# Performance work log

Hardware: AMD Instinct MI355X
Metric: run time of the kernel (lower is better)

The kernel has to match this reference:

```python
import math
import jax, jax.numpy as jnp
import numpy as np

B, N, H, D = 2, 2048, 16, 64


def _build_idx_table(seq_len, is_causal=True):
    """Fused hierarchical lookup table, faithful to
    build_hierarchical_index_lookup_table. Returns int32 [seq_len, log2(N)+1].
    Entries are (node_index + 1), negated if causally masked.
    Node numbering: leaves 0..N-1, then each level's parents appended;
    parent(i) = i // 2 + seq_len.
    """
    assert seq_len & (seq_len - 1) == 0
    total_nodes = 2 * seq_len - 1
    max_valid = total_nodes - 2  # root is never a neighbor
    level_num = int(math.log2(seq_len))
    total_cols = level_num + 1
    idx = np.ones((seq_len, total_cols), dtype=np.int32)
    n_cur = np.arange(seq_len, dtype=np.int64)
    idx[:, 0] = (n_cur + 1).astype(np.int32)  # self leaf
    for lvl in range(1, total_cols):
        if lvl == 1:
            n_next = n_cur ^ 1          # sibling leaf
            pair = n_cur
        else:
            pair = n_cur // 2 + seq_len  # parent node
            n_next = pair ^ 1            # uncle node
        valid = n_next <= max_valid
        val = n_next + 1
        if is_causal:
            should_mask = (pair < n_next) & valid
            val = np.where(should_mask, -val, val)
        idx[:, lvl] = np.where(valid, val.astype(np.int32), idx[:, lvl])
        n_cur = n_next
    return idx


IDX_TABLE = _build_idx_table(N, is_causal=True)  # [N, LEVELS]


def setup_inputs() -> dict:
    key = jax.random.key(0)
    kq, kk, kv = jax.random.split(key, 3)
    Q = jax.random.normal(kq, (B, N, H, D), dtype=jnp.float32)
    K = jax.random.normal(kk, (B, N, H, D), dtype=jnp.float32)
    V = jax.random.normal(kv, (B, N, H, D), dtype=jnp.float32)
    return {"Q": Q, "K": K, "V": V}


def _build_tree(K, V, scale):
    """Build the full binary-tree node set [B, 2N-1, H, D] for K and V.
    Each parent is a 3-way attention mix of {parent-mean, child0, child1}
    (build_parent_nodes semantics: fp32 online softmax with +1e-9 in denom),
    with the same weights applied to K and V values."""
    Ks, Vs = [K], [V]
    Kc, Vc = K, V
    while Kc.shape[1] > 1:  # trace-time loop over log2(N) levels
        K0, K1 = Kc[:, 0::2], Kc[:, 1::2]
        V0, V1 = Vc[:, 0::2], Vc[:, 1::2]
        Kp0 = 0.5 * (K0 + K1)  # initial parent K (query)
        Vp0 = 0.5 * (V0 + V1)
        s_self = jnp.sum(Kp0 * Kp0, axis=-1) * scale  # [B,P,H]
        s0 = jnp.sum(Kp0 * K0, axis=-1) * scale
        s1 = jnp.sum(Kp0 * K1, axis=-1) * scale
        m = jnp.maximum(s_self, jnp.maximum(s0, s1))
        e_s, e0, e1 = jnp.exp(s_self - m), jnp.exp(s0 - m), jnp.exp(s1 - m)
        denom = e_s + e0 + e1 + 1e-9
        ws, w0, w1 = (e_s / denom)[..., None], (e0 / denom)[..., None], (e1 / denom)[..., None]
        Kc = ws * Kp0 + w0 * K0 + w1 * K1
        Vc = ws * Vp0 + w0 * V0 + w1 * V1
        Ks.append(Kc)
        Vs.append(Vc)
    return jnp.concatenate(Ks, axis=1), jnp.concatenate(Vs, axis=1)


def reference(Q, K, V):
    b, n, h, d = Q.shape
    scale = 1.0 / math.sqrt(d)
    K_all, V_all = _build_tree(K, V, scale)  # [B, 2N-1, H, D]

    raw = jnp.asarray(IDX_TABLE)             # [N, L], sign-encoded
    nbr = jnp.abs(raw) - 1                   # neighbor node indices
    masked = raw < 0                         # causal mask

    Kg = jnp.take(K_all, nbr, axis=1)        # [B, N, L, H, D]
    Vg = jnp.take(V_all, nbr, axis=1)

    scores = jnp.einsum('bnhd,bnlhd->bnhl', Q, Kg) * scale
    scores = jnp.where(masked[None, :, None, :], -jnp.inf, scores)
    w = jax.nn.softmax(scores, axis=-1)      # [B, N, H, L]
    out = jnp.einsum('bnhl,bnlhd->bnhd', w, Vg)
    return out
```

## Files before the change

kernel.cpp:

```cpp
#include <hip/hip_runtime.h>

#define NSEQ   2048
#define HEADS  16
#define DIM    64
#define BATCH  2
#define SCALE  0.125f

#define WSSLOTS 2048
#define WSELEMS ((size_t)BATCH * WSSLOTS * HEADS * DIM)
#define ROWF4   (DIM / 4)
#define HSTRIDE (HEADS * ROWF4)

__device__ __forceinline__ int level_offset(int j) {
    return (j == 0) ? 0 : (2 * NSEQ - ((2 * NSEQ) >> j));
}

__device__ __forceinline__ float dot4(float4 a, float4 b) {
    return a.x * b.x + a.y * b.y + a.z * b.z + a.w * b.w;
}

__device__ __forceinline__ void reduce3_16(float& a, float& b, float& c) {
#pragma unroll
    for (int m = 1; m < 16; m <<= 1) {
        a += __shfl_xor(a, m, 64);
        b += __shfl_xor(b, m, 64);
        c += __shfl_xor(c, m, 64);
    }
}

__device__ __forceinline__ void make_parent4(float4 k0, float4 k1, float4 v0, float4 v1,
                                             float4& kc, float4& vc) {
    float4 kp, vp;
    kp.x = 0.5f * (k0.x + k1.x); kp.y = 0.5f * (k0.y + k1.y);
    kp.z = 0.5f * (k0.z + k1.z); kp.w = 0.5f * (k0.w + k1.w);
    vp.x = 0.5f * (v0.x + v1.x); vp.y = 0.5f * (v0.y + v1.y);
    vp.z = 0.5f * (v0.z + v1.z); vp.w = 0.5f * (v0.w + v1.w);
    float ss = dot4(kp, kp), sa = dot4(kp, k0), sb = dot4(kp, k1);
    reduce3_16(ss, sa, sb);
    ss *= SCALE; sa *= SCALE; sb *= SCALE;
    float mx = fmaxf(ss, fmaxf(sa, sb));
    float es = __expf(ss - mx), ea = __expf(sa - mx), eb = __expf(sb - mx);
    float inv = 1.0f / (es + ea + eb + 1e-9f);
    es *= inv; ea *= inv; eb *= inv;
    kc.x = es * kp.x + ea * k0.x + eb * k1.x;
    kc.y = es * kp.y + ea * k0.y + eb * k1.y;
    kc.z = es * kp.z + ea * k0.z + eb * k1.z;
    kc.w = es * kp.w + ea * k0.w + eb * k1.w;
    vc.x = es * vp.x + ea * v0.x + eb * v1.x;
    vc.y = es * vp.y + ea * v0.y + eb * v1.y;
    vc.z = es * vp.z + ea * v0.z + eb * v1.z;
    vc.w = es * vp.w + ea * v0.w + eb * v1.w;
}

__global__ __launch_bounds__(256) void tree_low(const float* __restrict__ K,
                                                const float* __restrict__ V,
                                                float* __restrict__ Kw,
                                                float* __restrict__ Vw) {
    __shared__ float4 Kb[96 * ROWF4];
    __shared__ float4 Vb[96 * ROWF4];
    int c  = blockIdx.x & 15;
    int bh = blockIdx.x >> 4;
    int h  = bh & 15;
    int b  = bh >> 4;
    int wave = threadIdx.x >> 6;
    int lane = threadIdx.x & 63;
    int g = lane >> 4;
    int t = lane & 15;

    const float4* K4 = (const float4*)K;
    const float4* V4 = (const float4*)V;
    float4* Kw4 = (float4*)Kw;
    float4* Vw4 = (float4*)Vw;

#pragma unroll
    for (int j = 1; j <= 7; ++j) {
        int P = 128 >> j;
        int curOff  = (j & 1) ? 0 : 64;
        int prevOff = (j & 1) ? 64 : 0;
        for (int i0 = 0; i0 < P; i0 += 16) {
            int p = i0 + wave * 4 + g;
            if (p < P) {
                float4 k0, k1, v0, v1;
                if (j == 1) {
                    int n0 = c * 128 + 2 * p;
                    const float4* Kr = K4 + ((size_t)(b * NSEQ + n0) * HEADS + h) * ROWF4;
                    const float4* Vr = V4 + ((size_t)(b * NSEQ + n0) * HEADS + h) * ROWF4;
                    k0 = Kr[t]; k1 = Kr[HSTRIDE + t];
                    v0 = Vr[t]; v1 = Vr[HSTRIDE + t];
                } else {
                    int s = (prevOff + 2 * p) * ROWF4 + t;
                    k0 = Kb[s]; k1 = Kb[s + ROWF4];
                    v0 = Vb[s]; v1 = Vb[s + ROWF4];
                }
                float4 kc, vc;
                make_parent4(k0, k1, v0, v1, kc, vc);
                Kb[(curOff + p) * ROWF4 + t] = kc;
                Vb[(curOff + p) * ROWF4 + t] = vc;
                int slot = level_offset(j) - NSEQ + c * P + p;
                size_t widx = ((size_t)(b * WSSLOTS + slot) * HEADS + h) * ROWF4 + t;
                Kw4[widx] = kc;
                Vw4[widx] = vc;
            }
        }
        __syncthreads();
    }
}

__global__ __launch_bounds__(256) void tree_top(float* __restrict__ Kw,
                                                float* __restrict__ Vw) {
    __shared__ float4 Kb[12 * ROWF4];
    __shared__ float4 Vb[12 * ROWF4];
    int h = blockIdx.x & 15;
    int b = blockIdx.x >> 4;
    int wave = threadIdx.x >> 6;
    int lane = threadIdx.x & 63;
    int g = lane >> 4, t = lane & 15;
    int p = wave * 4 + g;

    float4* Kw4 = (float4*)Kw;
    float4* Vw4 = (float4*)Vw;

    if (p < 8) {
        int cslot = level_offset(7) - NSEQ + 2 * p;
        size_t cb = ((size_t)(b * WSSLOTS + cslot) * HEADS + h) * ROWF4 + t;
        float4 k0 = Kw4[cb], k1 = Kw4[cb + HSTRIDE];
        float4 v0 = Vw4[cb], v1 = Vw4[cb + HSTRIDE];
        float4 kc, vc;
        make_parent4(k0, k1, v0, v1, kc, vc);
        Kb[p * ROWF4 + t] = kc;  Vb[p * ROWF4 + t] = vc;
        size_t widx = ((size_t)(b * WSSLOTS + level_offset(8) - NSEQ + p) * HEADS + h) * ROWF4 + t;
        Kw4[widx] = kc;  Vw4[widx] = vc;
    }
    __syncthreads();
    if (p < 4) {
        int s = (2 * p) * ROWF4 + t;
        float4 k0 = Kb[s], k1 = Kb[s + ROWF4];
        float4 v0 = Vb[s], v1 = Vb[s + ROWF4];
        float4 kc, vc;
        make_parent4(k0, k1, v0, v1, kc, vc);
        Kb[(8 + p) * ROWF4 + t] = kc;  Vb[(8 + p) * ROWF4 + t] = vc;
        size_t widx = ((size_t)(b * WSSLOTS + level_offset(9) - NSEQ + p) * HEADS + h) * ROWF4 + t;
        Kw4[widx] = kc;  Vw4[widx] = vc;
    }
    __syncthreads();
    if (p < 2) {
        int s = (8 + 2 * p) * ROWF4 + t;
        float4 k0 = Kb[s], k1 = Kb[s + ROWF4];
        float4 v0 = Vb[s], v1 = Vb[s + ROWF4];
        float4 kc, vc;
        make_parent4(k0, k1, v0, v1, kc, vc);
        size_t widx = ((size_t)(b * WSSLOTS + level_offset(10) - NSEQ + p) * HEADS + h) * ROWF4 + t;
        Kw4[widx] = kc;  Vw4[widx] = vc;
    }
}

__global__ __launch_bounds__(256) void attn(const float* __restrict__ Q,
                                            const float* __restrict__ K,
                                            const float* __restrict__ V,
                                            const float* __restrict__ Kw,
                                            const float* __restrict__ Vw,
                                            float* __restrict__ out) {
    int w = blockIdx.x * 4 + (threadIdx.x >> 6);
    int lane = threadIdx.x & 63;
    int g = lane >> 4;
    int t = lane & 15;
    int h = (w & 3) * 4 + g;
    int n = (w >> 2) & (NSEQ - 1);
    int b = w >> 13;

    const float4* Q4 = (const float4*)Q;
    const float4* K4 = (const float4*)K;
    const float4* V4 = (const float4*)V;
    const float4* Kw4 = (const float4*)Kw;
    const float4* Vw4 = (const float4*)Vw;

    size_t qrow = ((size_t)(b * NSEQ + n) * HEADS + h) * ROWF4;
    float4 q4 = Q4[qrow + t];

    unsigned active = 1u | (((unsigned)n & 0x7FFu) << 1);

    float s[12];
#pragma unroll
    for (int l = 0; l < 12; ++l) {
        int gn;
        if (l == 0) gn = n;
        else { int j = l - 1; gn = level_offset(j) + ((n >> j) ^ 1); }
        const float4* kp = (gn < NSEQ)
            ? K4  + ((size_t)(b * NSEQ   +  gn)         * HEADS + h) * ROWF4
            : Kw4 + ((size_t)(b * WSSLOTS + (gn - NSEQ)) * HEADS + h) * ROWF4;
        s[l] = dot4(q4, kp[t]);
    }
#pragma unroll
    for (int m = 1; m < 16; m <<= 1) {
#pragma unroll
        for (int l = 0; l < 12; ++l)
            s[l] += __shfl_xor(s[l], m, 64);
    }

    float mx = -3.402823466e+38f;
#pragma unroll
    for (int l = 0; l < 12; ++l) {
        s[l] *= SCALE;
        if (active & (1u << l)) mx = fmaxf(mx, s[l]);
    }
    float sum = 0.f;
#pragma unroll
    for (int l = 0; l < 12; ++l) {
        float e = (active & (1u << l)) ? __expf(s[l] - mx) : 0.f;
        s[l] = e;
        sum += e;
    }
    float inv = 1.0f / sum;

    float4 o = make_float4(0.f, 0.f, 0.f, 0.f);
#pragma unroll
    for (int l = 0; l < 12; ++l) {
        int gn;
        if (l == 0) gn = n;
        else { int j = l - 1; gn = level_offset(j) + ((n >> j) ^ 1); }
        const float4* vp = (gn < NSEQ)
            ? V4  + ((size_t)(b * NSEQ   +  gn)         * HEADS + h) * ROWF4
            : Vw4 + ((size_t)(b * WSSLOTS + (gn - NSEQ)) * HEADS + h) * ROWF4;
        float4 v = vp[t];
        o.x += s[l] * v.x; o.y += s[l] * v.y;
        o.z += s[l] * v.z; o.w += s[l] * v.w;
    }
    float4* O4 = (float4*)out;
    O4[qrow + t] = make_float4(o.x * inv, o.y * inv, o.z * inv, o.w * inv);
}

extern "C" void kernel_launch(void* const* d_in, const int* in_sizes, int n_in,
                              void* d_out, int out_size, void* d_ws, size_t ws_size,
                              hipStream_t stream) {
    const float* Q = (const float*)d_in[0];
    const float* K = (const float*)d_in[1];
    const float* V = (const float*)d_in[2];
    float* out = (float*)d_out;
    float* Kw = (float*)d_ws;
    float* Vw = Kw + WSELEMS;

    tree_low<<<BATCH * HEADS * 16, 256, 0, stream>>>(K, V, Kw, Vw);
    tree_top<<<BATCH * HEADS, 256, 0, stream>>>(Kw, Vw);
    attn<<<(BATCH * NSEQ * HEADS / 4) / 4, 256, 0, stream>>>(Q, K, V, Kw, Vw, out);
}
```

Baseline: 129.3 us.

## Fuse tree build and attention into one cooperative kernel with grid syncs

Replaces the three separate launches with one cooperative kernel of 1024 blocks that runs the low tree levels, the top tree levels and the attention phase, separated by grid-wide syncs. The low-level tree work is split into 64-leaf chunks instead of 128, so more blocks share it and the top phase covers more levels. Attention now gives each wave one sequence position and loops over the four head groups, computing neighbor row offsets once and reusing them. The aim is to remove launch gaps and inter-kernel idle time, at the cost of grid-sync overhead, a residency requirement for the cooperative launch, and a fallback path of three normal launches.

```diff
diff --git a/kernel.cpp b/kernel.cpp
--- a/kernel.cpp
+++ b/kernel.cpp
@@ -1,4 +1,7 @@
 #include <hip/hip_runtime.h>
+#include <hip/hip_cooperative_groups.h>
+
+namespace cg = cooperative_groups;
 
 #define NSEQ   2048
 #define HEADS  16
@@ -52,39 +55,31 @@
     vc.w = es * vp.w + ea * v0.w + eb * v1.w;
 }
 
-__global__ __launch_bounds__(256) void tree_low(const float* __restrict__ K,
-                                                const float* __restrict__ V,
-                                                float* __restrict__ Kw,
-                                                float* __restrict__ Vw) {
-    __shared__ float4 Kb[96 * ROWF4];
-    __shared__ float4 Vb[96 * ROWF4];
-    int c  = blockIdx.x & 15;
-    int bh = blockIdx.x >> 4;
-    int h  = bh & 15;
-    int b  = bh >> 4;
+__device__ __forceinline__ void phaseA(const float4* __restrict__ K4,
+                                       const float4* __restrict__ V4,
+                                       float4* __restrict__ Kw4,
+                                       float4* __restrict__ Vw4,
+                                       float4* Kb, float4* Vb, int bid) {
+    int c = bid & 31;
+    int h = (bid >> 5) & 15;
+    int b = bid >> 9;
     int wave = threadIdx.x >> 6;
     int lane = threadIdx.x & 63;
-    int g = lane >> 4;
-    int t = lane & 15;
-
-    const float4* K4 = (const float4*)K;
-    const float4* V4 = (const float4*)V;
-    float4* Kw4 = (float4*)Kw;
-    float4* Vw4 = (float4*)Vw;
-
-#pragma unroll
-    for (int j = 1; j <= 7; ++j) {
-        int P = 128 >> j;
-        int curOff  = (j & 1) ? 0 : 64;
-        int prevOff = (j & 1) ? 64 : 0;
+    int g = lane >> 4, t = lane & 15;
+
+#pragma unroll
+    for (int j = 1; j <= 6; ++j) {
+        int P = 64 >> j;
+        int curOff  = (j & 1) ? 0 : 32;
+        int prevOff = (j & 1) ? 32 : 0;
         for (int i0 = 0; i0 < P; i0 += 16) {
             int p = i0 + wave * 4 + g;
             if (p < P) {
                 float4 k0, k1, v0, v1;
                 if (j == 1) {
-                    int n0 = c * 128 + 2 * p;
-                    const float4* Kr = K4 + ((size_t)(b * NSEQ + n0) * HEADS + h) * ROWF4;
-                    const float4* Vr = V4 + ((size_t)(b * NSEQ + n0) * HEADS + h) * ROWF4;
+                    int n0 = c * 64 + 2 * p;
+                    const float4* Kr = K4 + ((size_t)((b * NSEQ + n0) * HEADS + h)) * ROWF4;
+                    const float4* Vr = V4 + ((size_t)((b * NSEQ + n0) * HEADS + h)) * ROWF4;
                     k0 = Kr[t]; k1 = Kr[HSTRIDE + t];
                     v0 = Vr[t]; v1 = Vr[HSTRIDE + t];
                 } else {
@@ -97,7 +92,7 @@
                 Kb[(curOff + p) * ROWF4 + t] = kc;
                 Vb[(curOff + p) * ROWF4 + t] = vc;
                 int slot = level_offset(j) - NSEQ + c * P + p;
-                size_t widx = ((size_t)(b * WSSLOTS + slot) * HEADS + h) * ROWF4 + t;
+                size_t widx = ((size_t)((b * WSSLOTS + slot) * HEADS + h)) * ROWF4 + t;
                 Kw4[widx] = kc;
                 Vw4[widx] = vc;
             }
@@ -106,127 +101,168 @@
     }
 }
 
-__global__ __launch_bounds__(256) void tree_top(float* __restrict__ Kw,
-                                                float* __restrict__ Vw) {
-    __shared__ float4 Kb[12 * ROWF4];
-    __shared__ float4 Vb[12 * ROWF4];
-    int h = blockIdx.x & 15;
-    int b = blockIdx.x >> 4;
-    int wave = threadIdx.x >> 6;
+__device__ __forceinline__ void phaseB(float4* __restrict__ Kw4,
+                                       float4* __restrict__ Vw4,
+                                       float4* Kb, float4* Vb, int bid) {
+    if (bid >= BATCH * HEADS) return;
+    int h = bid & 15, b = bid >> 4;
     int lane = threadIdx.x & 63;
     int g = lane >> 4, t = lane & 15;
-    int p = wave * 4 + g;
-
-    float4* Kw4 = (float4*)Kw;
-    float4* Vw4 = (float4*)Vw;
-
-    if (p < 8) {
-        int cslot = level_offset(7) - NSEQ + 2 * p;
-        size_t cb = ((size_t)(b * WSSLOTS + cslot) * HEADS + h) * ROWF4 + t;
+    int p = (threadIdx.x >> 6) * 4 + g;
+
+    {
+        size_t cb = ((size_t)((b * WSSLOTS + 1984 + 2 * p) * HEADS + h)) * ROWF4 + t;
         float4 k0 = Kw4[cb], k1 = Kw4[cb + HSTRIDE];
         float4 v0 = Vw4[cb], v1 = Vw4[cb + HSTRIDE];
         float4 kc, vc;
         make_parent4(k0, k1, v0, v1, kc, vc);
         Kb[p * ROWF4 + t] = kc;  Vb[p * ROWF4 + t] = vc;
-        size_t widx = ((size_t)(b * WSSLOTS + level_offset(8) - NSEQ + p) * HEADS + h) * ROWF4 + t;
-        Kw4[widx] = kc;  Vw4[widx] = vc;
+        size_t w = ((size_t)((b * WSSLOTS + 2016 + p) * HEADS + h)) * ROWF4 + t;
+        Kw4[w] = kc;  Vw4[w] = vc;
     }
     __syncthreads();
-    if (p < 4) {
+    if (p < 8) {
         int s = (2 * p) * ROWF4 + t;
         float4 k0 = Kb[s], k1 = Kb[s + ROWF4];
         float4 v0 = Vb[s], v1 = Vb[s + ROWF4];
         float4 kc, vc;
         make_parent4(k0, k1, v0, v1, kc, vc);
-        Kb[(8 + p) * ROWF4 + t] = kc;  Vb[(8 + p) * ROWF4 + t] = vc;
-        size_t widx = ((size_t)(b * WSSLOTS + level_offset(9) - NSEQ + p) * HEADS + h) * ROWF4 + t;
-        Kw4[widx] = kc;  Vw4[widx] = vc;
+        Kb[(16 + p) * ROWF4 + t] = kc;  Vb[(16 + p) * ROWF4 + t] = vc;
+        size_t w = ((size_t)((b * WSSLOTS + 2032 + p) * HEADS + h)) * ROWF4 + t;
+        Kw4[w] = kc;  Vw4[w] = vc;
+    }
+    __syncthreads();
+    if (p < 4) {
+        int s = (16 + 2 * p) * ROWF4 + t;
+        float4 k0 = Kb[s], k1 = Kb[s + ROWF4];
+        float4 v0 = Vb[s], v1 = Vb[s + ROWF4];
+        float4 kc, vc;
+        make_parent4(k0, k1, v0, v1, kc, vc);
+        Kb[(24 + p) * ROWF4 + t] = kc;  Vb[(24 + p) * ROWF4 + t] = vc;
+        size_t w = ((size_t)((b * WSSLOTS + 2040 + p) * HEADS + h)) * ROWF4 + t;
+        Kw4[w] = kc;  Vw4[w] = vc;
     }
     __syncthreads();
     if (p < 2) {
-        int s = (8 + 2 * p) * ROWF4 + t;
+        int s = (24 + 2 * p) * ROWF4 + t;
         float4 k0 = Kb[s], k1 = Kb[s + ROWF4];
         float4 v0 = Vb[s], v1 = Vb[s + ROWF4];
         float4 kc, vc;
         make_parent4(k0, k1, v0, v1, kc, vc);
-        size_t widx = ((size_t)(b * WSSLOTS + level_offset(10) - NSEQ + p) * HEADS + h) * ROWF4 + t;
-        Kw4[widx] = kc;  Vw4[widx] = vc;
-    }
-}
-
-__global__ __launch_bounds__(256) void attn(const float* __restrict__ Q,
-                                            const float* __restrict__ K,
-                                            const float* __restrict__ V,
-                                            const float* __restrict__ Kw,
-                                            const float* __restrict__ Vw,
-                                            float* __restrict__ out) {
-    int w = blockIdx.x * 4 + (threadIdx.x >> 6);
+        size_t w = ((size_t)((b * WSSLOTS + 2044 + p) * HEADS + h)) * ROWF4 + t;
+        Kw4[w] = kc;  Vw4[w] = vc;
+    }
+}
+
+__device__ __forceinline__ void phaseC(const float4* __restrict__ Q4,
+                                       const float4* __restrict__ K4,
+                                       const float4* __restrict__ V4,
+                                       const float4* __restrict__ Kw4,
+                                       const float4* __restrict__ Vw4,
+                                       float4* __restrict__ O4, int bid) {
+    int wv = bid * 4 + (threadIdx.x >> 6);
     int lane = threadIdx.x & 63;
-    int g = lane >> 4;
-    int t = lane & 15;
-    int h = (w & 3) * 4 + g;
-    int n = (w >> 2) & (NSEQ - 1);
-    int b = w >> 13;
-
+    int g = lane >> 4, t = lane & 15;
+    int n = wv & (NSEQ - 1);
+    int b = wv >> 11;
+
+    unsigned active = 1u | (((unsigned)n & 0x7FFu) << 1);
+
+    int row0 = (b * NSEQ + n) * HSTRIDE;
+    int row1 = (b * NSEQ + (n ^ 1)) * HSTRIDE;
+    int rowt[10];
+#pragma unroll
+    for (int l = 2; l < 12; ++l) {
+        int j = l - 1;
+        int gn = level_offset(j) + ((n >> j) ^ 1);
+        rowt[l - 2] = (b * WSSLOTS + (gn - NSEQ)) * HSTRIDE;
+    }
+
+    for (int hg = 0; hg < 4; ++hg) {
+        int hoff = (hg * 4 + g) * ROWF4 + t;
+        float4 q4 = Q4[row0 + hoff];
+
+        float s[12];
+        s[0] = dot4(q4, K4[row0 + hoff]);
+        s[1] = dot4(q4, K4[row1 + hoff]);
+#pragma unroll
+        for (int l = 2; l < 12; ++l) s[l] = dot4(q4, Kw4[rowt[l - 2] + hoff]);
+
+#pragma unroll
+        for (int m = 1; m < 16; m <<= 1) {
+#pragma unroll
+            for (int l = 0; l < 12; ++l) s[l] += __shfl_xor(s[l], m, 64);
+        }
+
+        float mx = -3.402823466e+38f;
+#pragma unroll
+        for (int l = 0; l < 12; ++l) {
+            s[l] *= SCALE;
+            if (active & (1u << l)) mx = fmaxf(mx, s[l]);
+        }
+        float sum = 0.f;
+#pragma unroll
+        for (int l = 0; l < 12; ++l) {
+            float e = (active & (1u << l)) ? __expf(s[l] - mx) : 0.f;
+            s[l] = e;
+            sum += e;
+        }
+        float inv = 1.0f / sum;
+
+        float4 o = make_float4(0.f, 0.f, 0.f, 0.f);
+        {
+            float4 v = V4[row0 + hoff];
+            o.x += s[0] * v.x; o.y += s[0] * v.y; o.z += s[0] * v.z; o.w += s[0] * v.w;
+            v = V4[row1 + hoff];
+            o.x += s[1] * v.x; o.y += s[1] * v.y; o.z += s[1] * v.z; o.w += s[1] * v.w;
+        }
+#pragma unroll
+        for (int l = 2; l < 12; ++l) {
+            float4 v = Vw4[rowt[l - 2] + hoff];
+            o.x += s[l] * v.x; o.y += s[l] * v.y; o.z += s[l] * v.z; o.w += s[l] * v.w;
+        }
+        O4[row0 + hoff] = make_float4(o.x * inv, o.y * inv, o.z * inv, o.w * inv);
+    }
+}
+
+__global__ __launch_bounds__(256, 4) void fused(const float* __restrict__ Q,
+                                                const float* __restrict__ K,
+                                                const float* __restrict__ V,
+                                                float* __restrict__ Kw,
+                                                float* __restrict__ Vw,
+                                                float* __restrict__ out) {
+    __shared__ float4 Kb[48 * ROWF4];
+    __shared__ float4 Vb[48 * ROWF4];
     const float4* Q4 = (const float4*)Q;
     const float4* K4 = (const float4*)K;
     const float4* V4 = (const float4*)V;
-    const float4* Kw4 = (const float4*)Kw;
-    const float4* Vw4 = (const float4*)Vw;
-
-    size_t qrow = ((size_t)(b * NSEQ + n) * HEADS + h) * ROWF4;
-    float4 q4 = Q4[qrow + t];
-
-    unsigned active = 1u | (((unsigned)n & 0x7FFu) << 1);
-
-    float s[12];
-#pragma unroll
-    for (int l = 0; l < 12; ++l) {
-        int gn;
-        if (l == 0) gn = n;
-        else { int j = l - 1; gn = level_offset(j) + ((n >> j) ^ 1); }
-        const float4* kp = (gn < NSEQ)
-            ? K4  + ((size_t)(b * NSEQ   +  gn)         * HEADS + h) * ROWF4
-            : Kw4 + ((size_t)(b * WSSLOTS + (gn - NSEQ)) * HEADS + h) * ROWF4;
-        s[l] = dot4(q4, kp[t]);
-    }
-#pragma unroll
-    for (int m = 1; m < 16; m <<= 1) {
-#pragma unroll
-        for (int l = 0; l < 12; ++l)
-            s[l] += __shfl_xor(s[l], m, 64);
-    }
-
-    float mx = -3.402823466e+38f;
-#pragma unroll
-    for (int l = 0; l < 12; ++l) {
-        s[l] *= SCALE;
-        if (active & (1u << l)) mx = fmaxf(mx, s[l]);
-    }
-    float sum = 0.f;
-#pragma unroll
-    for (int l = 0; l < 12; ++l) {
-        float e = (active & (1u << l)) ? __expf(s[l] - mx) : 0.f;
-        s[l] = e;
-        sum += e;
-    }
-    float inv = 1.0f / sum;
-
-    float4 o = make_float4(0.f, 0.f, 0.f, 0.f);
-#pragma unroll
-    for (int l = 0; l < 12; ++l) {
-        int gn;
-        if (l == 0) gn = n;
-        else { int j = l - 1; gn = level_offset(j) + ((n >> j) ^ 1); }
-        const float4* vp = (gn < NSEQ)
-            ? V4  + ((size_t)(b * NSEQ   +  gn)         * HEADS + h) * ROWF4
-            : Vw4 + ((size_t)(b * WSSLOTS + (gn - NSEQ)) * HEADS + h) * ROWF4;
-        float4 v = vp[t];
-        o.x += s[l] * v.x; o.y += s[l] * v.y;
-        o.z += s[l] * v.z; o.w += s[l] * v.w;
-    }
-    float4* O4 = (float4*)out;
-    O4[qrow + t] = make_float4(o.x * inv, o.y * inv, o.z * inv, o.w * inv);
+    float4* Kw4 = (float4*)Kw;
+    float4* Vw4 = (float4*)Vw;
+    float4* O4  = (float4*)out;
+    cg::grid_group grid = cg::this_grid();
+
+    phaseA(K4, V4, Kw4, Vw4, Kb, Vb, blockIdx.x);
+    grid.sync();
+    phaseB(Kw4, Vw4, Kb, Vb, blockIdx.x);
+    grid.sync();
+    phaseC(Q4, K4, V4, Kw4, Vw4, O4, blockIdx.x);
+}
+
+__global__ __launch_bounds__(256, 4) void treeA_k(const float* K, const float* V,
+                                                  float* Kw, float* Vw) {
+    __shared__ float4 Kb[48 * ROWF4];
+    __shared__ float4 Vb[48 * ROWF4];
+    phaseA((const float4*)K, (const float4*)V, (float4*)Kw, (float4*)Vw, Kb, Vb, blockIdx.x);
+}
+__global__ __launch_bounds__(256, 4) void treeB_k(float* Kw, float* Vw) {
+    __shared__ float4 Kb[48 * ROWF4];
+    __shared__ float4 Vb[48 * ROWF4];
+    phaseB((float4*)Kw, (float4*)Vw, Kb, Vb, blockIdx.x);
+}
+__global__ __launch_bounds__(256, 4) void attn_k(const float* Q, const float* K, const float* V,
+                                                 const float* Kw, const float* Vw, float* out) {
+    phaseC((const float4*)Q, (const float4*)K, (const float4*)V,
+           (const float4*)Kw, (const float4*)Vw, (float4*)out, blockIdx.x);
 }
 
 extern "C" void kernel_launch(void* const* d_in, const int* in_sizes, int n_in,
@@ -239,7 +275,14 @@
     float* Kw = (float*)d_ws;
     float* Vw = Kw + WSELEMS;
 
-    tree_low<<<BATCH * HEADS * 16, 256, 0, stream>>>(K, V, Kw, Vw);
-    tree_top<<<BATCH * HEADS, 256, 0, stream>>>(Kw, Vw);
-    attn<<<(BATCH * NSEQ * HEADS / 4) / 4, 256, 0, stream>>>(Q, K, V, Kw, Vw, out);
-}
+    void* args[] = { (void*)&Q, (void*)&K, (void*)&V,
+                     (void*)&Kw, (void*)&Vw, (void*)&out };
+    hipError_t e = hipLaunchCooperativeKernel(reinterpret_cast<void*>(fused),
+                                              dim3(1024), dim3(256), args, 0, stream);
+    if (e != hipSuccess) {
+        (void)hipGetLastError();
+        treeA_k<<<1024, 256, 0, stream>>>(K, V, Kw, Vw);
+        treeB_k<<<BATCH * HEADS, 256, 0, stream>>>(Kw, Vw);
+        attn_k<<<1024, 256, 0, stream>>>(Q, K, V, Kw, Vw, out);
+    }
+}
```

Measured after the change: 316.0 us. 144% more time.
